# Performance work log

Hardware: AMD Instinct MI355X
Metric: run time of the kernel (lower is better)

Reference implementation:

```python
import jax, jax.numpy as jnp
import numpy as np

THRESHOLD = 0.9
DECAY = 0.6


def setup_inputs() -> dict:
    key = jax.random.key(0)
    k1, k2, k3 = jax.random.split(key, 3)
    T, B, I, H, O = 100, 256, 784, 1024, 10
    # binary-ish spike input (rand fill, thresholded to emulate Poisson spikes)
    x = (jax.random.uniform(k1, (T, B, I)) < 0.3).astype(jnp.float32)
    W1 = 0.01 * jax.random.normal(k2, (I, H), dtype=jnp.float32)
    W2 = 0.01 * jax.random.normal(k3, (H, O), dtype=jnp.float32)
    return {"input_spikes_time": x, "W1": W1, "W2": W2}


def reference(input_spikes_time, W1, W2):
    T, B, _ = input_spikes_time.shape
    H = W1.shape[1]
    O = W2.shape[1]
    dt = input_spikes_time.dtype

    def lif(mem, current):
        # mem = mem*decay + I; spike if mem >= threshold; soft reset
        mem = mem * DECAY + current
        spikes = (mem >= THRESHOLD).astype(dt)
        mem = mem - spikes * THRESHOLD
        return mem, spikes

    def step(carry, x_t):
        mem1, mem2 = carry
        hidden_u = x_t @ W1                 # [B, H]
        mem1, hidden_spikes = lif(mem1, hidden_u)
        output_u = hidden_spikes @ W2       # [B, O]
        mem2, output_spikes = lif(mem2, output_u)
        return (mem1, mem2), (hidden_spikes, output_spikes)

    init = (jnp.zeros((B, H), dt), jnp.zeros((B, O), dt))
    _, (hidden_all, output_all) = jax.lax.scan(step, init, input_spikes_time)
    return hidden_all, output_all
```

## Files before the change

### kernel.cpp

```cpp
#include <hip/hip_runtime.h>
#include <hip/hip_bf16.h>

#define T_STEPS 100
#define BATCH   256
#define IN_DIM  784
#define HID_DIM 1024
#define OUT_DIM 10
#define M_ROWS  (T_STEPS * BATCH)
#define KPAD    800
#define DECAY   0.6f
#define THRESH  0.9f

typedef __attribute__((ext_vector_type(8))) short bf16x8;
typedef __attribute__((ext_vector_type(4))) float f32x4;

#define PACK8(dstp, v0, v1)                                                                        \
    {                                                                                              \
        unsigned int p0 = __builtin_amdgcn_perm(__builtin_bit_cast(unsigned int, (v0).y),          \
                                                __builtin_bit_cast(unsigned int, (v0).x), 0x07060302u); \
        unsigned int p1 = __builtin_amdgcn_perm(__builtin_bit_cast(unsigned int, (v0).w),          \
                                                __builtin_bit_cast(unsigned int, (v0).z), 0x07060302u); \
        unsigned int p2 = __builtin_amdgcn_perm(__builtin_bit_cast(unsigned int, (v1).y),          \
                                                __builtin_bit_cast(unsigned int, (v1).x), 0x07060302u); \
        unsigned int p3 = __builtin_amdgcn_perm(__builtin_bit_cast(unsigned int, (v1).w),          \
                                                __builtin_bit_cast(unsigned int, (v1).z), 0x07060302u); \
        *(uint4*)(dstp) = make_uint4(p0, p1, p2, p3);                                              \
    }

__global__ __launch_bounds__(256) void w1_split_T(const float* __restrict__ W1,
                                                  unsigned short* __restrict__ Th,
                                                  unsigned short* __restrict__ Tl) {
    __shared__ unsigned short lh[32][33];
    __shared__ unsigned short ll[32][33];
    const int nb = blockIdx.x * 32;
    const int kb = blockIdx.y * 32;
    const int t  = threadIdx.x;
    const int ln = t & 31, lk = t >> 5;
    #pragma unroll
    for (int i = 0; i < 4; ++i) {
        const int k = kb + lk + i * 8;
        const float w = (k < IN_DIM) ? W1[(size_t)k * HID_DIM + nb + ln] : 0.f;
        __hip_bfloat16 h = __float2bfloat16(w);
        float hf = __bfloat162float(h);
        __hip_bfloat16 l = __float2bfloat16(w - hf);
        lh[lk + i * 8][ln] = __builtin_bit_cast(unsigned short, h);
        ll[lk + i * 8][ln] = __builtin_bit_cast(unsigned short, l);
    }
    __syncthreads();
    const int o_n = t >> 3;
    const int o_k = (t & 7) * 4;
    ushort4 vh, vl;
    vh.x = lh[o_k + 0][o_n]; vh.y = lh[o_k + 1][o_n];
    vh.z = lh[o_k + 2][o_n]; vh.w = lh[o_k + 3][o_n];
    vl.x = ll[o_k + 0][o_n]; vl.y = ll[o_k + 1][o_n];
    vl.z = ll[o_k + 2][o_n]; vl.w = ll[o_k + 3][o_n];
    *(ushort4*)&Th[(size_t)(nb + o_n) * KPAD + kb + o_k] = vh;
    *(ushort4*)&Tl[(size_t)(nb + o_n) * KPAD + kb + o_k] = vl;
}

__global__ __launch_bounds__(256, 3) void gemm1_mfma(const float* __restrict__ X,
                                                     const unsigned short* __restrict__ Th,
                                                     const unsigned short* __restrict__ Tl,
                                                     float* __restrict__ C) {
    __shared__ unsigned short As[128 * 32];
    __shared__ unsigned short Bhs[128 * 32];
    __shared__ unsigned short Bls[128 * 32];

    const int tid = threadIdx.x;
    const int bid = blockIdx.x;
    const int xcd = bid & 7;
    const int j_  = bid >> 3;
    const int m0  = (xcd * 25 + (j_ >> 3)) * 128;
    const int n0  = (j_ & 7) * 128;

    const int lane = tid & 63, wv = tid >> 6;
    const int wm   = (wv & 1) * 64, wn = (wv >> 1) * 64;
    const int ml   = lane & 15, quad = lane >> 4;

    const int sr = tid >> 2;
    const int sc = tid & 3;
    const int f0 = (sr >> 1) & 3;
    const int w0 = sr * 32 + ((sc ^ f0) * 8);
    const int w1 = (sr + 64) * 32 + ((sc ^ f0) * 8);

    const float*          Xa = X  + (size_t)(m0 + sr)      * IN_DIM + sc * 8;
    const float*          Xb = X  + (size_t)(m0 + sr + 64) * IN_DIM + sc * 8;
    const unsigned short* Ha = Th + (size_t)(n0 + sr)      * KPAD   + sc * 8;
    const unsigned short* Hb = Th + (size_t)(n0 + sr + 64) * KPAD   + sc * 8;
    const unsigned short* La = Tl + (size_t)(n0 + sr)      * KPAD   + sc * 8;
    const unsigned short* Lb = Tl + (size_t)(n0 + sr + 64) * KPAD   + sc * 8;

    f32x4 acc[4][4];
    #pragma unroll
    for (int i = 0; i < 4; ++i)
        #pragma unroll
        for (int j = 0; j < 4; ++j)
            acc[i][j] = (f32x4){0.f, 0.f, 0.f, 0.f};

    float4 xa0 = *(const float4*)&Xa[0], xa1 = *(const float4*)&Xa[4];
    float4 xb0 = *(const float4*)&Xb[0], xb1 = *(const float4*)&Xb[4];
    uint4  vh0 = *(const uint4*)&Ha[0],  vh1 = *(const uint4*)&Hb[0];
    uint4  vl0 = *(const uint4*)&La[0],  vl1 = *(const uint4*)&Lb[0];
    PACK8(&As[w0], xa0, xa1);
    PACK8(&As[w1], xb0, xb1);
    *(uint4*)&Bhs[w0] = vh0;  *(uint4*)&Bhs[w1] = vh1;
    *(uint4*)&Bls[w0] = vl0;  *(uint4*)&Bls[w1] = vl1;
    __syncthreads();

    for (int it = 0; it < KPAD / 32; ++it) {
        bf16x8 af[4], bh[4], bl[4];
        #pragma unroll
        for (int i = 0; i < 4; ++i) {
            const int m = wm + i * 16 + ml;
            af[i] = *(const bf16x8*)&As[m * 32 + ((quad ^ ((m >> 1) & 3)) * 8)];
        }
        #pragma unroll
        for (int j = 0; j < 4; ++j) {
            const int n   = wn + j * 16 + ml;
            const int idx = n * 32 + ((quad ^ ((n >> 1) & 3)) * 8);
            bh[j] = *(const bf16x8*)&Bhs[idx];
            bl[j] = *(const bf16x8*)&Bls[idx];
        }

        const bool have_next = (it + 1 < KPAD / 32);
        if (have_next) {
            const int kt = (it + 1) * 32;
            const int c0 = kt + sc * 8;
            const bool v0 = (c0 < IN_DIM), v1 = (c0 + 4 < IN_DIM);
            xa0 = v0 ? *(const float4*)&Xa[kt]     : make_float4(0.f, 0.f, 0.f, 0.f);
            xa1 = v1 ? *(const float4*)&Xa[kt + 4] : make_float4(0.f, 0.f, 0.f, 0.f);
            xb0 = v0 ? *(const float4*)&Xb[kt]     : make_float4(0.f, 0.f, 0.f, 0.f);
            xb1 = v1 ? *(const float4*)&Xb[kt + 4] : make_float4(0.f, 0.f, 0.f, 0.f);
            vh0 = *(const uint4*)&Ha[kt];  vh1 = *(const uint4*)&Hb[kt];
            vl0 = *(const uint4*)&La[kt];  vl1 = *(const uint4*)&Lb[kt];
        }

        #pragma unroll
        for (int i = 0; i < 4; ++i)
            #pragma unroll
            for (int j = 0; j < 4; ++j) {
                acc[i][j] = __builtin_amdgcn_mfma_f32_16x16x32_bf16(af[i], bh[j], acc[i][j], 0, 0, 0);
                acc[i][j] = __builtin_amdgcn_mfma_f32_16x16x32_bf16(af[i], bl[j], acc[i][j], 0, 0, 0);
            }

        __syncthreads();
        if (have_next) {
            PACK8(&As[w0], xa0, xa1);
            PACK8(&As[w1], xb0, xb1);
            *(uint4*)&Bhs[w0] = vh0;  *(uint4*)&Bhs[w1] = vh1;
            *(uint4*)&Bls[w0] = vl0;  *(uint4*)&Bls[w1] = vl1;
            __syncthreads();
        }
    }

    #pragma unroll
    for (int i = 0; i < 4; ++i)
        #pragma unroll
        for (int j = 0; j < 4; ++j) {
            const int row = m0 + wm + i * 16 + quad * 4;
            const int col = n0 + wn + j * 16 + ml;
            #pragma unroll
            for (int r = 0; r < 4; ++r)
                C[(size_t)(row + r) * HID_DIM + col] = acc[i][j][r];
        }
}

__global__ __launch_bounds__(256) void lif1_fused(float* __restrict__ hid,
                                                  const float* __restrict__ W2,
                                                  float* __restrict__ outu) {
    const int idx = blockIdx.x * blockDim.x + threadIdx.x;
    float4* h4 = (float4*)hid;
    const int stride4 = (BATCH * HID_DIM) / 4;
    const int b  = (idx * 4) >> 10;
    const int h0 = (idx * 4) & 1023;

    float4 mem = make_float4(0.f, 0.f, 0.f, 0.f);
    float4 u[4];
    #pragma unroll
    for (int c = 0; c < 4; ++c) u[c] = h4[c * stride4 + idx];

    for (int t = 0; t < T_STEPS; t += 4) {
        float4 nu[4];
        if (t + 4 < T_STEPS) {
            #pragma unroll
            for (int c = 0; c < 4; ++c) nu[c] = h4[(t + 4 + c) * stride4 + idx];
        }
        #pragma unroll
        for (int c = 0; c < 4; ++c) {
            float4 uu = u[c];
            float4 s;
            mem.x = mem.x * DECAY + uu.x; s.x = (mem.x >= THRESH) ? 1.f : 0.f; mem.x -= s.x * THRESH;
            mem.y = mem.y * DECAY + uu.y; s.y = (mem.y >= THRESH) ? 1.f : 0.f; mem.y -= s.y * THRESH;
            mem.z = mem.z * DECAY + uu.z; s.z = (mem.z >= THRESH) ? 1.f : 0.f; mem.z -= s.z * THRESH;
            mem.w = mem.w * DECAY + uu.w; s.w = (mem.w >= THRESH) ? 1.f : 0.f; mem.w -= s.w * THRESH;
            h4[(t + c) * stride4 + idx] = s;
            if (s.x + s.y + s.z + s.w > 0.f) {
                float* od = outu + (size_t)(t + c) * (BATCH * OUT_DIM) + b * OUT_DIM;
                #pragma unroll
                for (int e = 0; e < 4; ++e) {
                    const float sv = (&s.x)[e];
                    if (sv != 0.f) {
                        const float* w = W2 + (size_t)(h0 + e) * OUT_DIM;
                        #pragma unroll
                        for (int o = 0; o < OUT_DIM; ++o) atomicAdd(&od[o], w[o]);
                    }
                }
            }
        }
        #pragma unroll
        for (int c = 0; c < 4; ++c) u[c] = nu[c];
    }
}

__global__ __launch_bounds__(256) void lif2(float* __restrict__ outp) {
    const int n = blockIdx.x * blockDim.x + threadIdx.x;
    const int stride = BATCH * OUT_DIM;
    if (n >= stride) return;
    float mem = 0.f;
    float u[4];
    #pragma unroll
    for (int c = 0; c < 4; ++c) u[c] = outp[c * stride + n];
    for (int t = 0; t < T_STEPS; t += 4) {
        float nu[4];
        if (t + 4 < T_STEPS) {
            #pragma unroll
            for (int c = 0; c < 4; ++c) nu[c] = outp[(t + 4 + c) * stride + n];
        }
        #pragma unroll
        for (int c = 0; c < 4; ++c) {
            mem = mem * DECAY + u[c];
            float s = (mem >= THRESH) ? 1.f : 0.f;
            mem -= s * THRESH;
            outp[(t + c) * stride + n] = s;
        }
        #pragma unroll
        for (int c = 0; c < 4; ++c) u[c] = nu[c];
    }
}

extern "C" void kernel_launch(void* const* d_in, const int* in_sizes, int n_in,
                              void* d_out, int out_size, void* d_ws, size_t ws_size,
                              hipStream_t stream) {
    const float* x  = (const float*)d_in[0];
    const float* W1 = (const float*)d_in[1];
    const float* W2 = (const float*)d_in[2];
    float* out  = (float*)d_out;
    float* hid  = out;
    float* outu = out + (size_t)M_ROWS * HID_DIM;

    unsigned short* Th = (unsigned short*)d_ws;
    unsigned short* Tl = Th + (size_t)HID_DIM * KPAD;

    dim3 gt(HID_DIM / 32, KPAD / 32);
    w1_split_T<<<gt, 256, 0, stream>>>(W1, Th, Tl);

    hipMemsetAsync(outu, 0, (size_t)M_ROWS * OUT_DIM * sizeof(float), stream);

    gemm1_mfma<<<1600, 256, 0, stream>>>(x, Th, Tl, hid);

    lif1_fused<<<(BATCH * HID_DIM / 4) / 256, 256, 0, stream>>>(hid, W2, outu);

    lif2<<<(BATCH * OUT_DIM + 255) / 256, 256, 0, stream>>>(outu);
}
```

Before: 303.2 us.

## Deepen gemm1 global-load prefetch to two stages with register ping-pong

Restructures the gemm1 main loop so global loads of X are issued two K-tiles ahead using ping-pong register sets, and the B loads for tile it+2 are issued right after the shared-memory store. This gives each global load more time to land before it is needed, hiding memory latency. It raises register use, so launch bounds drop the minimum blocks per CU from 3 to 2, which may lower occupancy.

```diff
diff --git a/kernel.cpp b/kernel.cpp
--- a/kernel.cpp
+++ b/kernel.cpp
@@ -8,6 +8,7 @@
 #define OUT_DIM 10
 #define M_ROWS  (T_STEPS * BATCH)
 #define KPAD    800
+#define NITER   (KPAD / 32)
 #define DECAY   0.6f
 #define THRESH  0.9f
 
@@ -58,7 +59,57 @@
     *(ushort4*)&Tl[(size_t)(nb + o_n) * KPAD + kb + o_k] = vl;
 }
 
-__global__ __launch_bounds__(256, 3) void gemm1_mfma(const float* __restrict__ X,
+#define LOADA(KT, S)                                                        \
+    {                                                                       \
+        const int  _c0 = (KT) + sc * 8;                                     \
+        const bool _v0 = (_c0 < IN_DIM), _v1 = (_c0 + 4 < IN_DIM);          \
+        S[0] = _v0 ? *(const float4*)&Xa[(KT)]     : f4z;                   \
+        S[1] = _v1 ? *(const float4*)&Xa[(KT) + 4] : f4z;                   \
+        S[2] = _v0 ? *(const float4*)&Xb[(KT)]     : f4z;                   \
+        S[3] = _v1 ? *(const float4*)&Xb[(KT) + 4] : f4z;                   \
+    }
+
+#define LOADB(KT)                                                           \
+    {                                                                       \
+        pb0 = *(const uint4*)&Ha[(KT)]; pb1 = *(const uint4*)&Hb[(KT)];     \
+        pb2 = *(const uint4*)&La[(KT)]; pb3 = *(const uint4*)&Lb[(KT)];     \
+    }
+
+#define BODY(IT, SCUR, SNXT)                                                \
+    {                                                                       \
+        bf16x8 af[4], bh[4], bl[4];                                         \
+        _Pragma("unroll")                                                   \
+        for (int i = 0; i < 4; ++i) {                                       \
+            const int m = wm + i * 16 + ml;                                 \
+            af[i] = *(const bf16x8*)&As[m * 32 + ((quad ^ ((m >> 1) & 3)) * 8)]; \
+        }                                                                   \
+        _Pragma("unroll")                                                   \
+        for (int j = 0; j < 4; ++j) {                                       \
+            const int n   = wn + j * 16 + ml;                               \
+            const int idx = n * 32 + ((quad ^ ((n >> 1) & 3)) * 8);         \
+            bh[j] = *(const bf16x8*)&Bhs[idx];                              \
+            bl[j] = *(const bf16x8*)&Bls[idx];                              \
+        }                                                                   \
+        if ((IT) + 2 < NITER) LOADA(((IT) + 2) * 32, SNXT);                 \
+        _Pragma("unroll")                                                   \
+        for (int i = 0; i < 4; ++i)                                         \
+            _Pragma("unroll")                                               \
+            for (int j = 0; j < 4; ++j) {                                   \
+                acc[i][j] = __builtin_amdgcn_mfma_f32_16x16x32_bf16(af[i], bh[j], acc[i][j], 0, 0, 0); \
+                acc[i][j] = __builtin_amdgcn_mfma_f32_16x16x32_bf16(af[i], bl[j], acc[i][j], 0, 0, 0); \
+            }                                                               \
+        __syncthreads();                                                    \
+        if ((IT) + 1 < NITER) {                                             \
+            PACK8(&As[w0], SCUR[0], SCUR[1]);                               \
+            PACK8(&As[w1], SCUR[2], SCUR[3]);                               \
+            *(uint4*)&Bhs[w0] = pb0;  *(uint4*)&Bhs[w1] = pb1;              \
+            *(uint4*)&Bls[w0] = pb2;  *(uint4*)&Bls[w1] = pb3;              \
+            if ((IT) + 2 < NITER) LOADB(((IT) + 2) * 32);                   \
+            __syncthreads();                                                \
+        }                                                                   \
+    }
+
+__global__ __launch_bounds__(256, 2) void gemm1_mfma(const float* __restrict__ X,
                                                      const unsigned short* __restrict__ Th,
                                                      const unsigned short* __restrict__ Tl,
                                                      float* __restrict__ C) {
@@ -90,6 +141,10 @@
     const unsigned short* La = Tl + (size_t)(n0 + sr)      * KPAD   + sc * 8;
     const unsigned short* Lb = Tl + (size_t)(n0 + sr + 64) * KPAD   + sc * 8;
 
+    const float4 f4z = make_float4(0.f, 0.f, 0.f, 0.f);
+    float4 sa[4], sb[4];
+    uint4  pb0, pb1, pb2, pb3;
+
     f32x4 acc[4][4];
     #pragma unroll
     for (int i = 0; i < 4; ++i)
@@ -97,60 +152,19 @@
         for (int j = 0; j < 4; ++j)
             acc[i][j] = (f32x4){0.f, 0.f, 0.f, 0.f};
 
-    float4 xa0 = *(const float4*)&Xa[0], xa1 = *(const float4*)&Xa[4];
-    float4 xb0 = *(const float4*)&Xb[0], xb1 = *(const float4*)&Xb[4];
-    uint4  vh0 = *(const uint4*)&Ha[0],  vh1 = *(const uint4*)&Hb[0];
-    uint4  vl0 = *(const uint4*)&La[0],  vl1 = *(const uint4*)&Lb[0];
-    PACK8(&As[w0], xa0, xa1);
-    PACK8(&As[w1], xb0, xb1);
-    *(uint4*)&Bhs[w0] = vh0;  *(uint4*)&Bhs[w1] = vh1;
-    *(uint4*)&Bls[w0] = vl0;  *(uint4*)&Bls[w1] = vl1;
+    LOADA(0, sa);
+    LOADB(0);
+    PACK8(&As[w0], sa[0], sa[1]);
+    PACK8(&As[w1], sa[2], sa[3]);
+    *(uint4*)&Bhs[w0] = pb0;  *(uint4*)&Bhs[w1] = pb1;
+    *(uint4*)&Bls[w0] = pb2;  *(uint4*)&Bls[w1] = pb3;
+    LOADA(32, sb);
+    LOADB(32);
     __syncthreads();
 
-    for (int it = 0; it < KPAD / 32; ++it) {
-        bf16x8 af[4], bh[4], bl[4];
-        #pragma unroll
-        for (int i = 0; i < 4; ++i) {
-            const int m = wm + i * 16 + ml;
-            af[i] = *(const bf16x8*)&As[m * 32 + ((quad ^ ((m >> 1) & 3)) * 8)];
-        }
-        #pragma unroll
-        for (int j = 0; j < 4; ++j) {
-            const int n   = wn + j * 16 + ml;
-            const int idx = n * 32 + ((quad ^ ((n >> 1) & 3)) * 8);
-            bh[j] = *(const bf16x8*)&Bhs[idx];
-            bl[j] = *(const bf16x8*)&Bls[idx];
-        }
-
-        const bool have_next = (it + 1 < KPAD / 32);
-        if (have_next) {
-            const int kt = (it + 1) * 32;
-            const int c0 = kt + sc * 8;
-            const bool v0 = (c0 < IN_DIM), v1 = (c0 + 4 < IN_DIM);
-            xa0 = v0 ? *(const float4*)&Xa[kt]     : make_float4(0.f, 0.f, 0.f, 0.f);
-            xa1 = v1 ? *(const float4*)&Xa[kt + 4] : make_float4(0.f, 0.f, 0.f, 0.f);
-            xb0 = v0 ? *(const float4*)&Xb[kt]     : make_float4(0.f, 0.f, 0.f, 0.f);
-            xb1 = v1 ? *(const float4*)&Xb[kt + 4] : make_float4(0.f, 0.f, 0.f, 0.f);
-            vh0 = *(const uint4*)&Ha[kt];  vh1 = *(const uint4*)&Hb[kt];
-            vl0 = *(const uint4*)&La[kt];  vl1 = *(const uint4*)&Lb[kt];
-        }
-
-        #pragma unroll
-        for (int i = 0; i < 4; ++i)
-            #pragma unroll
-            for (int j = 0; j < 4; ++j) {
-                acc[i][j] = __builtin_amdgcn_mfma_f32_16x16x32_bf16(af[i], bh[j], acc[i][j], 0, 0, 0);
-                acc[i][j] = __builtin_amdgcn_mfma_f32_16x16x32_bf16(af[i], bl[j], acc[i][j], 0, 0, 0);
-            }
-
-        __syncthreads();
-        if (have_next) {
-            PACK8(&As[w0], xa0, xa1);
-            PACK8(&As[w1], xb0, xb1);
-            *(uint4*)&Bhs[w0] = vh0;  *(uint4*)&Bhs[w1] = vh1;
-            *(uint4*)&Bls[w0] = vl0;  *(uint4*)&Bls[w1] = vl1;
-            __syncthreads();
-        }
+    for (int it = 0; it < NITER; it += 2) {
+        BODY(it, sb, sa);
+        if (it + 1 < NITER) BODY(it + 1, sa, sb);
     }
 
     #pragma unroll
```

New measurement: 445.3 us. 1.47x slower.

## Double-buffer LDS tiles in GEMM and deepen LIF prefetch to two steps

Applied to the files above, without the earlier changes.

The GEMM kernel now keeps two LDS buffers for the A, B-high and B-low tiles and writes the next tile into the alternate buffer, which removes one __syncthreads per K iteration. The LIF kernel prefetches hidden currents two 4-step groups ahead instead of one, giving the global loads more time to land. The cost is doubled LDS use (48KB per block), which may cut the 3-blocks-per-CU occupancy target, plus more live registers in the LIF kernel.

```diff
diff --git a/kernel.cpp b/kernel.cpp
--- a/kernel.cpp
+++ b/kernel.cpp
@@ -8,6 +8,7 @@
 #define OUT_DIM 10
 #define M_ROWS  (T_STEPS * BATCH)
 #define KPAD    800
+#define NITER   (KPAD / 32)
 #define DECAY   0.6f
 #define THRESH  0.9f
 
@@ -58,13 +59,33 @@
     *(ushort4*)&Tl[(size_t)(nb + o_n) * KPAD + kb + o_k] = vl;
 }
 
+#define LOADTILE(KT)                                                        \
+    {                                                                       \
+        const int  _c0 = (KT) + sc * 8;                                     \
+        const bool _v0 = _c0 < IN_DIM, _v1 = (_c0 + 4) < IN_DIM;            \
+        xa0 = _v0 ? *(const float4*)&Xa[(KT)]     : f4z;                    \
+        xa1 = _v1 ? *(const float4*)&Xa[(KT) + 4] : f4z;                    \
+        xb0 = _v0 ? *(const float4*)&Xb[(KT)]     : f4z;                    \
+        xb1 = _v1 ? *(const float4*)&Xb[(KT) + 4] : f4z;                    \
+        vh0 = *(const uint4*)&Ha[(KT)];  vh1 = *(const uint4*)&Hb[(KT)];    \
+        vl0 = *(const uint4*)&La[(KT)];  vl1 = *(const uint4*)&Lb[(KT)];    \
+    }
+
+#define STORETILE(BUF)                                                      \
+    {                                                                       \
+        PACK8(&As[BUF][w0], xa0, xa1);                                      \
+        PACK8(&As[BUF][w1], xb0, xb1);                                      \
+        *(uint4*)&Bhs[BUF][w0] = vh0;  *(uint4*)&Bhs[BUF][w1] = vh1;        \
+        *(uint4*)&Bls[BUF][w0] = vl0;  *(uint4*)&Bls[BUF][w1] = vl1;        \
+    }
+
 __global__ __launch_bounds__(256, 3) void gemm1_mfma(const float* __restrict__ X,
                                                      const unsigned short* __restrict__ Th,
                                                      const unsigned short* __restrict__ Tl,
                                                      float* __restrict__ C) {
-    __shared__ unsigned short As[128 * 32];
-    __shared__ unsigned short Bhs[128 * 32];
-    __shared__ unsigned short Bls[128 * 32];
+    __shared__ unsigned short As[2][128 * 32];
+    __shared__ unsigned short Bhs[2][128 * 32];
+    __shared__ unsigned short Bls[2][128 * 32];
 
     const int tid = threadIdx.x;
     const int bid = blockIdx.x;
@@ -90,6 +111,10 @@
     const unsigned short* La = Tl + (size_t)(n0 + sr)      * KPAD   + sc * 8;
     const unsigned short* Lb = Tl + (size_t)(n0 + sr + 64) * KPAD   + sc * 8;
 
+    const float4 f4z = make_float4(0.f, 0.f, 0.f, 0.f);
+    float4 xa0, xa1, xb0, xb1;
+    uint4  vh0, vh1, vl0, vl1;
+
     f32x4 acc[4][4];
     #pragma unroll
     for (int i = 0; i < 4; ++i)
@@ -97,43 +122,29 @@
         for (int j = 0; j < 4; ++j)
             acc[i][j] = (f32x4){0.f, 0.f, 0.f, 0.f};
 
-    float4 xa0 = *(const float4*)&Xa[0], xa1 = *(const float4*)&Xa[4];
-    float4 xb0 = *(const float4*)&Xb[0], xb1 = *(const float4*)&Xb[4];
-    uint4  vh0 = *(const uint4*)&Ha[0],  vh1 = *(const uint4*)&Hb[0];
-    uint4  vl0 = *(const uint4*)&La[0],  vl1 = *(const uint4*)&Lb[0];
-    PACK8(&As[w0], xa0, xa1);
-    PACK8(&As[w1], xb0, xb1);
-    *(uint4*)&Bhs[w0] = vh0;  *(uint4*)&Bhs[w1] = vh1;
-    *(uint4*)&Bls[w0] = vl0;  *(uint4*)&Bls[w1] = vl1;
+    LOADTILE(0);
+    STORETILE(0);
     __syncthreads();
 
-    for (int it = 0; it < KPAD / 32; ++it) {
+    for (int it = 0; it < NITER; ++it) {
+        const int cur = it & 1;
+
         bf16x8 af[4], bh[4], bl[4];
         #pragma unroll
         for (int i = 0; i < 4; ++i) {
             const int m = wm + i * 16 + ml;
-            af[i] = *(const bf16x8*)&As[m * 32 + ((quad ^ ((m >> 1) & 3)) * 8)];
+            af[i] = *(const bf16x8*)&As[cur][m * 32 + ((quad ^ ((m >> 1) & 3)) * 8)];
         }
         #pragma unroll
         for (int j = 0; j < 4; ++j) {
             const int n   = wn + j * 16 + ml;
             const int idx = n * 32 + ((quad ^ ((n >> 1) & 3)) * 8);
-            bh[j] = *(const bf16x8*)&Bhs[idx];
-            bl[j] = *(const bf16x8*)&Bls[idx];
-        }
-
-        const bool have_next = (it + 1 < KPAD / 32);
-        if (have_next) {
-            const int kt = (it + 1) * 32;
-            const int c0 = kt + sc * 8;
-            const bool v0 = (c0 < IN_DIM), v1 = (c0 + 4 < IN_DIM);
-            xa0 = v0 ? *(const float4*)&Xa[kt]     : make_float4(0.f, 0.f, 0.f, 0.f);
-            xa1 = v1 ? *(const float4*)&Xa[kt + 4] : make_float4(0.f, 0.f, 0.f, 0.f);
-            xb0 = v0 ? *(const float4*)&Xb[kt]     : make_float4(0.f, 0.f, 0.f, 0.f);
-            xb1 = v1 ? *(const float4*)&Xb[kt + 4] : make_float4(0.f, 0.f, 0.f, 0.f);
-            vh0 = *(const uint4*)&Ha[kt];  vh1 = *(const uint4*)&Hb[kt];
-            vl0 = *(const uint4*)&La[kt];  vl1 = *(const uint4*)&Lb[kt];
-        }
+            bh[j] = *(const bf16x8*)&Bhs[cur][idx];
+            bl[j] = *(const bf16x8*)&Bls[cur][idx];
+        }
+
+        const bool have_next = (it + 1 < NITER);
+        if (have_next) LOADTILE((it + 1) * 32);
 
         #pragma unroll
         for (int i = 0; i < 4; ++i)
@@ -143,12 +154,8 @@
                 acc[i][j] = __builtin_amdgcn_mfma_f32_16x16x32_bf16(af[i], bl[j], acc[i][j], 0, 0, 0);
             }
 
-        __syncthreads();
         if (have_next) {
-            PACK8(&As[w0], xa0, xa1);
-            PACK8(&As[w1], xb0, xb1);
-            *(uint4*)&Bhs[w0] = vh0;  *(uint4*)&Bhs[w1] = vh1;
-            *(uint4*)&Bls[w0] = vl0;  *(uint4*)&Bls[w1] = vl1;
+            STORETILE(cur ^ 1);
             __syncthreads();
         }
     }
@@ -175,16 +182,13 @@
     const int h0 = (idx * 4) & 1023;
 
     float4 mem = make_float4(0.f, 0.f, 0.f, 0.f);
-    float4 u[4];
+    float4 u[4], v[4];
     #pragma unroll
     for (int c = 0; c < 4; ++c) u[c] = h4[c * stride4 + idx];
+    #pragma unroll
+    for (int c = 0; c < 4; ++c) v[c] = h4[(4 + c) * stride4 + idx];
 
     for (int t = 0; t < T_STEPS; t += 4) {
-        float4 nu[4];
-        if (t + 4 < T_STEPS) {
-            #pragma unroll
-            for (int c = 0; c < 4; ++c) nu[c] = h4[(t + 4 + c) * stride4 + idx];
-        }
         #pragma unroll
         for (int c = 0; c < 4; ++c) {
             float4 uu = u[c];
@@ -208,7 +212,11 @@
             }
         }
         #pragma unroll
-        for (int c = 0; c < 4; ++c) u[c] = nu[c];
+        for (int c = 0; c < 4; ++c) u[c] = v[c];
+        if (t + 8 < T_STEPS) {
+            #pragma unroll
+            for (int c = 0; c < 4; ++c) v[c] = h4[(t + 8 + c) * stride4 + idx];
+        }
     }
 }
 
```

New measurement: 423.9 us. +39.8%, slower.
